# Kernel tuning notes

Hardware: AMD Instinct MI355X
Metric: run time of the kernel (lower is better)

The kernel has to match this reference:

```python
import jax, jax.numpy as jnp
import numpy as np

N_NODES = 50000
N_EDGES = 800000
IN_DIM = 128
HIDDEN = 128
OUT_DIM = 128


def setup_inputs() -> dict:
    key = jax.random.key(0)
    k1, k2, k3, k4, k5, k6 = jax.random.split(key, 6)
    X = jax.random.normal(k1, (N_NODES, IN_DIM), dtype=jnp.float32)
    W0 = jax.random.normal(k2, (HIDDEN, IN_DIM), dtype=jnp.float32) * (1.0 / np.sqrt(IN_DIM))
    W1 = jax.random.normal(k3, (OUT_DIM, HIDDEN), dtype=jnp.float32) * (1.0 / np.sqrt(HIDDEN))
    norm = jax.random.uniform(k4, (N_EDGES,), dtype=jnp.float32)
    src = jax.random.randint(k5, (N_EDGES,), 0, N_NODES, dtype=jnp.int32)
    dst = jax.random.randint(k6, (N_EDGES,), 0, N_NODES, dtype=jnp.int32)
    return {"X": X, "W0": W0, "W1": W1, "norm": norm, "src": src, "dst": dst}


def _propagate(S, src, dst, norm, n_nodes):
    # gather-scale-scatter: Z[dst] += S[src] * norm   (SpMM-style)
    msg = S[src] * norm[:, None]  # [E, d]
    return jax.ops.segment_sum(msg, dst, num_segments=n_nodes)


def reference(X, W0, W1, norm, src, dst):
    n = X.shape[0]
    # layer 1: linear (nn.Linear stores W as [out,in], so x @ W.T) + propagate + relu
    S0 = X @ W0.T                       # [N, hidden]
    H = jax.nn.relu(_propagate(S0, src, dst, norm, n))
    # dropout p=0.5 -> identity in eval mode (reference baseline)
    S1 = H @ W1.T                       # [N, out]
    Z = _propagate(S1, src, dst, norm, n)
    return (Z, H)
```

## Files before the change

kernel.cpp:

```cpp
#include <hip/hip_runtime.h>

#define DIM 128
#define NB 196

typedef __attribute__((ext_vector_type(8))) short bf16x8_t;
typedef __attribute__((ext_vector_type(4))) float f32x4_t;

__device__ __forceinline__ short f2bf(float f) {
    unsigned u = __float_as_uint(f);
    u += 0x7FFFu + ((u >> 16) & 1u);
    return (short)(u >> 16);
}
__device__ __forceinline__ float bf2f(short s) {
    return __uint_as_float(((unsigned)(unsigned short)s) << 16);
}

__global__ void cvt_f32_bf16(const float* __restrict__ in, short* __restrict__ out, int n) {
    int i = (blockIdx.x * 256 + threadIdx.x) * 8;
    if (i < n) {
        float4 a = *(const float4*)(in + i);
        float4 b = *(const float4*)(in + i + 4);
        bf16x8_t o;
        o[0] = f2bf(a.x); o[1] = f2bf(a.y); o[2] = f2bf(a.z); o[3] = f2bf(a.w);
        o[4] = f2bf(b.x); o[5] = f2bf(b.y); o[6] = f2bf(b.z); o[7] = f2bf(b.w);
        *(bf16x8_t*)(out + i) = o;
    }
}

__global__ __launch_bounds__(256) void bucket_count(const int* __restrict__ dst,
                                                    int* __restrict__ bcount, int E) {
    __shared__ int hist[NB];
    int t = threadIdx.x;
    for (int b = t; b < NB; b += 256) hist[b] = 0;
    __syncthreads();
    int idx = (blockIdx.x * 256 + t) * 4;
    if (idx + 3 < E) {
        int4 d = *(const int4*)(dst + idx);
        atomicAdd(&hist[d.x >> 8], 1);
        atomicAdd(&hist[d.y >> 8], 1);
        atomicAdd(&hist[d.z >> 8], 1);
        atomicAdd(&hist[d.w >> 8], 1);
    } else {
        for (int k = idx; k < E; k++) atomicAdd(&hist[dst[k] >> 8], 1);
    }
    __syncthreads();
    for (int b = t; b < NB; b += 256) {
        int c = hist[b];
        if (c) atomicAdd(&bcount[b], c);
    }
}

__global__ __launch_bounds__(256) void bucket_scan(const int* __restrict__ bcount,
                                                   int* __restrict__ boffs,
                                                   int* __restrict__ bcursor) {
    __shared__ int ws_[4];
    int t = threadIdx.x;
    int v = (t < NB) ? bcount[t] : 0;
    int lane = t & 63, w = t >> 6;
    int s = v;
    #pragma unroll
    for (int o = 1; o < 64; o <<= 1) { int x = __shfl_up(s, o, 64); if (lane >= o) s += x; }
    if (lane == 63) ws_[w] = s;
    __syncthreads();
    int wpref = 0;
    for (int k = 0; k < w; k++) wpref += ws_[k];
    int incl = wpref + s;
    int excl = incl - v;
    if (t < NB) { boffs[t] = excl; bcursor[t] = excl; }
    if (t == 255) boffs[NB] = incl;
}

#define SC_VPT 16
__global__ __launch_bounds__(256) void bucket_scatter(const int* __restrict__ src,
                                                      const int* __restrict__ dst,
                                                      const float* __restrict__ norm,
                                                      int* __restrict__ bcursor,
                                                      int2* __restrict__ binned, int E) {
    __shared__ int hist[NB];
    __shared__ int base[NB];
    int t = threadIdx.x;
    for (int b = t; b < NB; b += 256) hist[b] = 0;
    __syncthreads();

    int e0 = blockIdx.x * (256 * SC_VPT);
    int bkts[SC_VPT];
    int pack[SC_VPT];
    int nrm[SC_VPT];
    #pragma unroll
    for (int k = 0; k < SC_VPT; k++) {
        int e = e0 + k * 256 + t;
        if (e < E) {
            int d = dst[e];
            bkts[k] = d >> 8;
            pack[k] = ((d & 255) << 24) | src[e];
            nrm[k]  = __float_as_int(norm[e]);
            atomicAdd(&hist[bkts[k]], 1);
        } else bkts[k] = -1;
    }
    __syncthreads();
    for (int b = t; b < NB; b += 256) {
        int c = hist[b];
        base[b] = c ? atomicAdd(&bcursor[b], c) : 0;
        hist[b] = 0;
    }
    __syncthreads();
    #pragma unroll
    for (int k = 0; k < SC_VPT; k++) {
        if (bkts[k] >= 0) {
            int pos = base[bkts[k]] + atomicAdd(&hist[bkts[k]], 1);
            binned[pos] = make_int2(pack[k], nrm[k]);
        }
    }
}

__global__ __launch_bounds__(1024) void bucket_csr(const int2* __restrict__ binned,
                                                   const int* __restrict__ boffs,
                                                   int* __restrict__ offs,
                                                   int2* __restrict__ edges, int n) {
    __shared__ int hist[256];
    __shared__ int ws_[4];
    int b   = blockIdx.x;
    int beg = boffs[b];
    int end = boffs[b + 1];
    int t   = threadIdx.x;
    if (t < 256) hist[t] = 0;
    __syncthreads();
    for (int i = beg + t; i < end; i += 1024)
        atomicAdd(&hist[(unsigned)binned[i].x >> 24], 1);
    __syncthreads();
    int v = (t < 256) ? hist[t] : 0;
    int lane = t & 63, w = t >> 6;
    int s = v;
    #pragma unroll
    for (int o = 1; o < 64; o <<= 1) { int x = __shfl_up(s, o, 64); if (lane >= o) s += x; }
    if (t < 256 && lane == 63) ws_[w] = s;
    __syncthreads();
    int wpref = 0;
    if (t < 256) for (int k = 0; k < w; k++) wpref += ws_[k];
    int excl = wpref + s - v;
    __syncthreads();
    if (t < 256) {
        hist[t] = beg + excl;
        int idx = b * 256 + t;
        if (idx <= n) offs[idx] = beg + excl;
    }
    __syncthreads();
    for (int i = beg + t; i < end; i += 1024) {
        int2 pr = binned[i];
        unsigned p = (unsigned)pr.x;
        int pos = atomicAdd(&hist[p >> 24], 1);
        edges[pos] = make_int2((int)(p & 0xFFFFFF), pr.y);
    }
}


__global__ __launch_bounds__(256) void gemm_mfma(const float* __restrict__ A,
                                                 const short* __restrict__ Wbf,
                                                 short* __restrict__ Cbf, int n) {
    int wave = threadIdx.x >> 6;
    int lane = threadIdx.x & 63;
    int l16  = lane & 15;
    int quad = lane >> 4;
    int r0 = blockIdx.x * 64 + wave * 16;

    int arow = r0 + l16;
    if (arow >= n) arow = n - 1;
    const float* Ar = A + (size_t)arow * DIM + quad * 8;

    bf16x8_t fa[4];
    #pragma unroll
    for (int kk = 0; kk < 4; kk++) {
        float4 x0 = *(const float4*)(Ar + kk * 32);
        float4 x1 = *(const float4*)(Ar + kk * 32 + 4);
        bf16x8_t f;
        f[0] = f2bf(x0.x); f[1] = f2bf(x0.y); f[2] = f2bf(x0.z); f[3] = f2bf(x0.w);
        f[4] = f2bf(x1.x); f[5] = f2bf(x1.y); f[6] = f2bf(x1.z); f[7] = f2bf(x1.w);
        fa[kk] = f;
    }

    #pragma unroll
    for (int ct = 0; ct < 8; ct++) {
        const short* Wr = Wbf + (size_t)(ct * 16 + l16) * DIM + quad * 8;
        f32x4_t acc = {0.f, 0.f, 0.f, 0.f};
        #pragma unroll
        for (int kk = 0; kk < 4; kk++) {
            bf16x8_t fb = *(const bf16x8_t*)(Wr + kk * 32);
            acc = __builtin_amdgcn_mfma_f32_16x16x32_bf16(fa[kk], fb, acc, 0, 0, 0);
        }
        #pragma unroll
        for (int j = 0; j < 4; j++) {
            int row = r0 + quad * 4 + j;
            if (row < n) Cbf[(size_t)row * DIM + ct * 16 + l16] = f2bf(acc[j]);
        }
    }
}


__global__ __launch_bounds__(256) void propagate_kernel(const short* __restrict__ Sbf,
                                                        const int* __restrict__ offs,
                                                        const int2* __restrict__ edges,
                                                        float* __restrict__ out,
                                                        int n, int do_relu) {
    int node = blockIdx.x * 4 + (threadIdx.x >> 6);
    if (node >= n) return;
    int lane = threadIdx.x & 63;
    int q   = lane >> 4;
    int l16 = lane & 15;
    int beg = offs[node];
    int end = offs[node + 1];

    float acc[8] = {};
    int i = beg + q;
    for (; i + 4 < end; i += 8) {
        int2 e0 = edges[i];
        int2 e1 = edges[i + 4];
        bf16x8_t v0 = *(const bf16x8_t*)(Sbf + (size_t)e0.x * DIM + l16 * 8);
        bf16x8_t v1 = *(const bf16x8_t*)(Sbf + (size_t)e1.x * DIM + l16 * 8);
        float n0 = __int_as_float(e0.y);
        float n1 = __int_as_float(e1.y);
        #pragma unroll
        for (int j = 0; j < 8; j++) acc[j] += n0 * bf2f(v0[j]);
        #pragma unroll
        for (int j = 0; j < 8; j++) acc[j] += n1 * bf2f(v1[j]);
    }
    for (; i < end; i += 4) {
        int2 e = edges[i];
        bf16x8_t v = *(const bf16x8_t*)(Sbf + (size_t)e.x * DIM + l16 * 8);
        float nv = __int_as_float(e.y);
        #pragma unroll
        for (int j = 0; j < 8; j++) acc[j] += nv * bf2f(v[j]);
    }

    #pragma unroll
    for (int j = 0; j < 8; j++) {
        acc[j] += __shfl_xor(acc[j], 16, 64);
        acc[j] += __shfl_xor(acc[j], 32, 64);
    }
    if (q == 0) {
        if (do_relu) {
            #pragma unroll
            for (int j = 0; j < 8; j++) acc[j] = fmaxf(acc[j], 0.f);
        }
        float4 o0 = make_float4(acc[0], acc[1], acc[2], acc[3]);
        float4 o1 = make_float4(acc[4], acc[5], acc[6], acc[7]);
        float* row = out + (size_t)node * DIM + l16 * 8;
        *(float4*)row       = o0;
        *(float4*)(row + 4) = o1;
    }
}


extern "C" void kernel_launch(void* const* d_in, const int* in_sizes, int n_in,
                              void* d_out, int out_size, void* d_ws, size_t ws_size,
                              hipStream_t stream) {
    const float* X    = (const float*)d_in[0];
    const float* W0   = (const float*)d_in[1];
    const float* W1   = (const float*)d_in[2];
    const float* norm = (const float*)d_in[3];
    const int*   src  = (const int*)d_in[4];
    const int*   dst  = (const int*)d_in[5];

    const int N = in_sizes[0] / DIM;
    const int E = in_sizes[3];

    float* Z = (float*)d_out;
    float* H = (float*)d_out + (size_t)N * DIM;

    char* ws = (char*)d_ws;
    short* Sbf    = (short*)ws;
    size_t off    = (size_t)N * DIM * sizeof(short);
    short* Wbf0   = (short*)(ws + off); off += DIM * DIM * sizeof(short);
    short* Wbf1   = (short*)(ws + off); off += DIM * DIM * sizeof(short);
    int*   offs   = (int*)(ws + off); off += ((size_t)(N + 1) * 4 + 255) / 256 * 256;
    int*   bcount = (int*)(ws + off); off += 1024;
    int*   boffs  = (int*)(ws + off); off += 1024;
    int*   bcursor= (int*)(ws + off); off += 1024;
    int2*  binned = (int2*)(ws + off); off += (size_t)E * 8;
    int2*  edges  = (int2*)(ws + off); off += (size_t)E * 8;

    cvt_f32_bf16<<<(DIM * DIM + 2047) / 2048, 256, 0, stream>>>(W0, Wbf0, DIM * DIM);
    cvt_f32_bf16<<<(DIM * DIM + 2047) / 2048, 256, 0, stream>>>(W1, Wbf1, DIM * DIM);

    hipMemsetAsync(bcount, 0, NB * sizeof(int), stream);
    bucket_count<<<(E / 4 + 255) / 256, 256, 0, stream>>>(dst, bcount, E);
    bucket_scan<<<1, 256, 0, stream>>>(bcount, boffs, bcursor);
    bucket_scatter<<<(E + 256 * SC_VPT - 1) / (256 * SC_VPT), 256, 0, stream>>>(
        src, dst, norm, bcursor, binned, E);
    bucket_csr<<<NB, 1024, 0, stream>>>(binned, boffs, offs, edges, N);

    const int gemm_grid = (N + 63) / 64;
    const int prop_grid = (N + 3) / 4;

    gemm_mfma<<<gemm_grid, 256, 0, stream>>>(X, Wbf0, Sbf, N);
    propagate_kernel<<<prop_grid, 256, 0, stream>>>(Sbf, offs, edges, H, N, 1);

    gemm_mfma<<<gemm_grid, 256, 0, stream>>>(H, Wbf1, Sbf, N);
    propagate_kernel<<<prop_grid, 256, 0, stream>>>(Sbf, offs, edges, Z, N, 0);
}
```

Baseline: 237.6 us.

## Use fixed-capacity buckets to drop count pass, unroll propagate, nontemporal edge loads

```diff
diff --git a/kernel.cpp b/kernel.cpp
--- a/kernel.cpp
+++ b/kernel.cpp
@@ -2,6 +2,7 @@
 
 #define DIM 128
 #define NB 196
+#define BCAP 6144
 
 typedef __attribute__((ext_vector_type(8))) short bf16x8_t;
 typedef __attribute__((ext_vector_type(4))) float f32x4_t;
@@ -14,60 +15,21 @@
 __device__ __forceinline__ float bf2f(short s) {
     return __uint_as_float(((unsigned)(unsigned short)s) << 16);
 }
-
-__global__ void cvt_f32_bf16(const float* __restrict__ in, short* __restrict__ out, int n) {
+__device__ __forceinline__ int2 ldnt_edge(const int2* p) {
+    long long v = __builtin_nontemporal_load((const long long*)p);
+    return make_int2((int)(unsigned)(v & 0xffffffffLL), (int)(v >> 32));
+}
+
+__global__ void cvt_w_bf16(const float* __restrict__ W0, const float* __restrict__ W1,
+                           short* __restrict__ Wbf) {
     int i = (blockIdx.x * 256 + threadIdx.x) * 8;
-    if (i < n) {
-        float4 a = *(const float4*)(in + i);
-        float4 b = *(const float4*)(in + i + 4);
-        bf16x8_t o;
-        o[0] = f2bf(a.x); o[1] = f2bf(a.y); o[2] = f2bf(a.z); o[3] = f2bf(a.w);
-        o[4] = f2bf(b.x); o[5] = f2bf(b.y); o[6] = f2bf(b.z); o[7] = f2bf(b.w);
-        *(bf16x8_t*)(out + i) = o;
-    }
-}
-
-__global__ __launch_bounds__(256) void bucket_count(const int* __restrict__ dst,
-                                                    int* __restrict__ bcount, int E) {
-    __shared__ int hist[NB];
-    int t = threadIdx.x;
-    for (int b = t; b < NB; b += 256) hist[b] = 0;
-    __syncthreads();
-    int idx = (blockIdx.x * 256 + t) * 4;
-    if (idx + 3 < E) {
-        int4 d = *(const int4*)(dst + idx);
-        atomicAdd(&hist[d.x >> 8], 1);
-        atomicAdd(&hist[d.y >> 8], 1);
-        atomicAdd(&hist[d.z >> 8], 1);
-        atomicAdd(&hist[d.w >> 8], 1);
-    } else {
-        for (int k = idx; k < E; k++) atomicAdd(&hist[dst[k] >> 8], 1);
-    }
-    __syncthreads();
-    for (int b = t; b < NB; b += 256) {
-        int c = hist[b];
-        if (c) atomicAdd(&bcount[b], c);
-    }
-}
-
-__global__ __launch_bounds__(256) void bucket_scan(const int* __restrict__ bcount,
-                                                   int* __restrict__ boffs,
-                                                   int* __restrict__ bcursor) {
-    __shared__ int ws_[4];
-    int t = threadIdx.x;
-    int v = (t < NB) ? bcount[t] : 0;
-    int lane = t & 63, w = t >> 6;
-    int s = v;
-    #pragma unroll
-    for (int o = 1; o < 64; o <<= 1) { int x = __shfl_up(s, o, 64); if (lane >= o) s += x; }
-    if (lane == 63) ws_[w] = s;
-    __syncthreads();
-    int wpref = 0;
-    for (int k = 0; k < w; k++) wpref += ws_[k];
-    int incl = wpref + s;
-    int excl = incl - v;
-    if (t < NB) { boffs[t] = excl; bcursor[t] = excl; }
-    if (t == 255) boffs[NB] = incl;
+    const float* in = (i < DIM * DIM) ? (W0 + i) : (W1 + (i - DIM * DIM));
+    float4 a = *(const float4*)in;
+    float4 b = *(const float4*)(in + 4);
+    bf16x8_t o;
+    o[0] = f2bf(a.x); o[1] = f2bf(a.y); o[2] = f2bf(a.z); o[3] = f2bf(a.w);
+    o[4] = f2bf(b.x); o[5] = f2bf(b.y); o[6] = f2bf(b.z); o[7] = f2bf(b.w);
+    *(bf16x8_t*)(Wbf + i) = o;
 }
 
 #define SC_VPT 16
@@ -100,7 +62,7 @@
     __syncthreads();
     for (int b = t; b < NB; b += 256) {
         int c = hist[b];
-        base[b] = c ? atomicAdd(&bcursor[b], c) : 0;
+        base[b] = b * BCAP + (c ? atomicAdd(&bcursor[b], c) : 0);
         hist[b] = 0;
     }
     __syncthreads();
@@ -111,6 +73,24 @@
             binned[pos] = make_int2(pack[k], nrm[k]);
         }
     }
+}
+
+__global__ __launch_bounds__(256) void bucket_scan(const int* __restrict__ bcount,
+                                                   int* __restrict__ boffs) {
+    __shared__ int ws_[4];
+    int t = threadIdx.x;
+    int v = (t < NB) ? bcount[t] : 0;
+    int lane = t & 63, w = t >> 6;
+    int s = v;
+    #pragma unroll
+    for (int o = 1; o < 64; o <<= 1) { int x = __shfl_up(s, o, 64); if (lane >= o) s += x; }
+    if (lane == 63) ws_[w] = s;
+    __syncthreads();
+    int wpref = 0;
+    for (int k = 0; k < w; k++) wpref += ws_[k];
+    int incl = wpref + s;
+    if (t < NB) boffs[t] = incl - v;
+    if (t == 255) boffs[NB] = incl;
 }
 
 __global__ __launch_bounds__(1024) void bucket_csr(const int2* __restrict__ binned,
@@ -119,14 +99,15 @@
                                                    int2* __restrict__ edges, int n) {
     __shared__ int hist[256];
     __shared__ int ws_[4];
-    int b   = blockIdx.x;
-    int beg = boffs[b];
-    int end = boffs[b + 1];
-    int t   = threadIdx.x;
+    int b    = blockIdx.x;
+    int beg  = boffs[b];
+    int cnt  = boffs[b + 1] - beg;
+    int ibase= b * BCAP;
+    int t    = threadIdx.x;
     if (t < 256) hist[t] = 0;
     __syncthreads();
-    for (int i = beg + t; i < end; i += 1024)
-        atomicAdd(&hist[(unsigned)binned[i].x >> 24], 1);
+    for (int i = t; i < cnt; i += 1024)
+        atomicAdd(&hist[(unsigned)binned[ibase + i].x >> 24], 1);
     __syncthreads();
     int v = (t < 256) ? hist[t] : 0;
     int lane = t & 63, w = t >> 6;
@@ -145,8 +126,8 @@
         if (idx <= n) offs[idx] = beg + excl;
     }
     __syncthreads();
-    for (int i = beg + t; i < end; i += 1024) {
-        int2 pr = binned[i];
+    for (int i = t; i < cnt; i += 1024) {
+        int2 pr = binned[ibase + i];
         unsigned p = (unsigned)pr.x;
         int pos = atomicAdd(&hist[p >> 24], 1);
         edges[pos] = make_int2((int)(p & 0xFFFFFF), pr.y);
@@ -211,20 +192,30 @@
 
     float acc[8] = {};
     int i = beg + q;
-    for (; i + 4 < end; i += 8) {
-        int2 e0 = edges[i];
-        int2 e1 = edges[i + 4];
+    for (; i + 12 < end; i += 16) {
+        int2 e0 = ldnt_edge(&edges[i]);
+        int2 e1 = ldnt_edge(&edges[i + 4]);
+        int2 e2 = ldnt_edge(&edges[i + 8]);
+        int2 e3 = ldnt_edge(&edges[i + 12]);
         bf16x8_t v0 = *(const bf16x8_t*)(Sbf + (size_t)e0.x * DIM + l16 * 8);
         bf16x8_t v1 = *(const bf16x8_t*)(Sbf + (size_t)e1.x * DIM + l16 * 8);
+        bf16x8_t v2 = *(const bf16x8_t*)(Sbf + (size_t)e2.x * DIM + l16 * 8);
+        bf16x8_t v3 = *(const bf16x8_t*)(Sbf + (size_t)e3.x * DIM + l16 * 8);
         float n0 = __int_as_float(e0.y);
         float n1 = __int_as_float(e1.y);
+        float n2 = __int_as_float(e2.y);
+        float n3 = __int_as_float(e3.y);
         #pragma unroll
         for (int j = 0; j < 8; j++) acc[j] += n0 * bf2f(v0[j]);
         #pragma unroll
         for (int j = 0; j < 8; j++) acc[j] += n1 * bf2f(v1[j]);
+        #pragma unroll
+        for (int j = 0; j < 8; j++) acc[j] += n2 * bf2f(v2[j]);
+        #pragma unroll
+        for (int j = 0; j < 8; j++) acc[j] += n3 * bf2f(v3[j]);
     }
     for (; i < end; i += 4) {
-        int2 e = edges[i];
+        int2 e = ldnt_edge(&edges[i]);
         bf16x8_t v = *(const bf16x8_t*)(Sbf + (size_t)e.x * DIM + l16 * 8);
         float nv = __int_as_float(e.y);
         #pragma unroll
@@ -241,11 +232,11 @@
             #pragma unroll
             for (int j = 0; j < 8; j++) acc[j] = fmaxf(acc[j], 0.f);
         }
-        float4 o0 = make_float4(acc[0], acc[1], acc[2], acc[3]);
-        float4 o1 = make_float4(acc[4], acc[5], acc[6], acc[7]);
+        f32x4_t o0 = {acc[0], acc[1], acc[2], acc[3]};
+        f32x4_t o1 = {acc[4], acc[5], acc[6], acc[7]};
         float* row = out + (size_t)node * DIM + l16 * 8;
-        *(float4*)row       = o0;
-        *(float4*)(row + 4) = o1;
+        __builtin_nontemporal_store(o0, (f32x4_t*)row);
+        __builtin_nontemporal_store(o1, (f32x4_t*)(row + 4));
     }
 }
 
@@ -269,23 +260,20 @@
     char* ws = (char*)d_ws;
     short* Sbf    = (short*)ws;
     size_t off    = (size_t)N * DIM * sizeof(short);
-    short* Wbf0   = (short*)(ws + off); off += DIM * DIM * sizeof(short);
-    short* Wbf1   = (short*)(ws + off); off += DIM * DIM * sizeof(short);
+    short* Wbf0   = (short*)(ws + off); off += 2 * DIM * DIM * sizeof(short);
+    short* Wbf1   = Wbf0 + DIM * DIM;
     int*   offs   = (int*)(ws + off); off += ((size_t)(N + 1) * 4 + 255) / 256 * 256;
-    int*   bcount = (int*)(ws + off); off += 1024;
+    int*   bcursor= (int*)(ws + off); off += 1024;
     int*   boffs  = (int*)(ws + off); off += 1024;
-    int*   bcursor= (int*)(ws + off); off += 1024;
-    int2*  binned = (int2*)(ws + off); off += (size_t)E * 8;
+    int2*  binned = (int2*)(ws + off); off += (size_t)NB * BCAP * 8;
     int2*  edges  = (int2*)(ws + off); off += (size_t)E * 8;
 
-    cvt_f32_bf16<<<(DIM * DIM + 2047) / 2048, 256, 0, stream>>>(W0, Wbf0, DIM * DIM);
-    cvt_f32_bf16<<<(DIM * DIM + 2047) / 2048, 256, 0, stream>>>(W1, Wbf1, DIM * DIM);
-
-    hipMemsetAsync(bcount, 0, NB * sizeof(int), stream);
-    bucket_count<<<(E / 4 + 255) / 256, 256, 0, stream>>>(dst, bcount, E);
-    bucket_scan<<<1, 256, 0, stream>>>(bcount, boffs, bcursor);
+    cvt_w_bf16<<<(2 * DIM * DIM) / (256 * 8), 256, 0, stream>>>(W0, W1, Wbf0);
+
+    hipMemsetAsync(bcursor, 0, NB * sizeof(int), stream);
     bucket_scatter<<<(E + 256 * SC_VPT - 1) / (256 * SC_VPT), 256, 0, stream>>>(
         src, dst, norm, bcursor, binned, E);
+    bucket_scan<<<1, 256, 0, stream>>>(bcursor, boffs);
     bucket_csr<<<NB, 1024, 0, stream>>>(binned, boffs, offs, edges, N);
 
     const int gemm_grid = (N + 63) / 64;
```

Measured after the change: 230.0 us. 1.03x faster.
